# Performance work log

Measured on AMD Instinct MI355X. Metric: run time of the kernel, lower is better.

## Reference

```python
import jax, jax.numpy as jnp
import numpy as np

N, F, E = 10000, 128, 640000
HID_RO = 64


def setup_inputs() -> dict:
    key = jax.random.key(0)
    ks = jax.random.split(key, 16)
    s = 1.0 / np.sqrt(F)
    inp = {
        'h': jax.random.normal(ks[0], (N, F), jnp.float32),
        'src_idx': jax.random.randint(ks[1], (E,), 0, N, jnp.int32),
        'dst_idx': jax.random.randint(ks[2], (E,), 0, N, jnp.int32),
        # message-creation MLP (F -> F -> F)
        'W1': jax.random.normal(ks[3], (F, F), jnp.float32) * s,
        'b1': jnp.zeros((F,), jnp.float32),
        'W2': jax.random.normal(ks[4], (F, F), jnp.float32) * s,
        'b2': jnp.zeros((F,), jnp.float32),
        # attention aggregation kernels
        'node_kernel': jax.random.normal(ks[5], (F, F), jnp.float32) * s,
        'attn_kernel': jax.random.normal(ks[6], (2 * F, 1), jnp.float32) * s,
        # feed-forward update (agg + h -> new h)
        'Wu': jax.random.normal(ks[7], (2 * F, F), jnp.float32) * s,
        'bu': jnp.zeros((F,), jnp.float32),
        # readout MLP (F -> 64 -> 1)
        'Wr1': jax.random.normal(ks[8], (F, HID_RO), jnp.float32) * s,
        'br1': jnp.zeros((HID_RO,), jnp.float32),
        'Wr2': jax.random.normal(ks[9], (HID_RO, 1), jnp.float32) * (1.0 / np.sqrt(HID_RO)),
        'br2': jnp.zeros((1,), jnp.float32),
    }
    return inp


def reference(h, src_idx, dst_idx, W1, b1, W2, b2, node_kernel, attn_kernel,
              Wu, bu, Wr1, br1, Wr2, br2):
    n = h.shape[0]
    # per-edge gather + message-creation NN  [E, F]
    h_src = h[src_idx]
    m = jax.nn.relu(h_src @ W1 + b1) @ W2 + b2
    # attention aggregation (GAT-style): transform messages, score vs dst state
    wh = m @ node_kernel                      # [E, F]
    h_dst = h[dst_idx]                        # [E, F]
    e = jax.nn.leaky_relu(jnp.concatenate([wh, h_dst], axis=-1) @ attn_kernel,
                          negative_slope=0.2)[:, 0]  # [E]
    # per-destination segment softmax (numerically stable)
    e_max = jax.ops.segment_max(e, dst_idx, num_segments=n)
    ex = jnp.exp(e - e_max[dst_idx])
    denom = jax.ops.segment_sum(ex, dst_idx, num_segments=n)
    alpha = ex / (denom[dst_idx] + 1e-9)
    # scatter-reduce weighted messages into destination states  [N, F]
    agg = jax.ops.segment_sum(m * alpha[:, None], dst_idx, num_segments=n)
    # feed-forward update
    h_new = jax.nn.relu(jnp.concatenate([agg, h], axis=-1) @ Wu + bu)
    # readout MLP -> per-node scalar
    out = jax.nn.relu(h_new @ Wr1 + br1) @ Wr2 + br2  # [N, 1]
    return out
```

## Files before the change

### kernel.cpp

```cpp
#include <hip/hip_runtime.h>
#include <hip/hip_bf16.h>
#include <hip/hip_fp16.h>

#define F 128
#define HID 64
#define KMAX 4
#define DEG_CAP 256
#define NTM 16
#define NTU 16
#define CHUNK_LOG 13
#define CHUNK (1 << CHUNK_LOG)


__global__ __launch_bounds__(256) void fused_front(
    const int* __restrict__ dst, unsigned short* __restrict__ cnt,
    unsigned short* __restrict__ rank,
    int e, int n, int histBlocks,
    const float* __restrict__ h,
    const float* __restrict__ W1, const float* __restrict__ b1,
    const float* __restrict__ W2, const float* __restrict__ b2,
    const float* __restrict__ nk, const float* __restrict__ attn,
    __half* __restrict__ Mh, float* __restrict__ p, float* __restrict__ q)
{
    __shared__ __align__(16) int lhist[10240];
    int tid = threadIdx.x;

    if ((int)blockIdx.x < histBlocks) {
        int n4 = n >> 2;
        int4* lh4 = (int4*)lhist;
        for (int i = tid; i < n4; i += 256) lh4[i] = make_int4(0, 0, 0, 0);
        for (int i = (n4 << 2) + tid; i < n; i += 256) lhist[i] = 0;
        __syncthreads();

        int base = (int)blockIdx.x << CHUNK_LOG;
        int lim = min(e - base, CHUNK);
        int lim4 = lim >> 2;
        const int4* d4 = (const int4*)(dst + base);
        for (int k = tid; k < lim4; k += 256) {
            int4 dv = d4[k];
            ushort4 rv;
            rv.x = (unsigned short)atomicAdd(&lhist[dv.x], 1);
            rv.y = (unsigned short)atomicAdd(&lhist[dv.y], 1);
            rv.z = (unsigned short)atomicAdd(&lhist[dv.z], 1);
            rv.w = (unsigned short)atomicAdd(&lhist[dv.w], 1);
            *(ushort4*)&rank[base + 4 * k] = rv;
        }
        for (int k = (lim4 << 2) + tid; k < lim; k += 256)
            rank[base + k] = (unsigned short)atomicAdd(&lhist[dst[base + k]], 1);
        __syncthreads();

        unsigned int* crow = (unsigned int*)(cnt + (size_t)blockIdx.x * n);
        int nh = n >> 1;
        for (int i = tid; i < nh; i += 256) {
            unsigned int v = ((unsigned int)lhist[2 * i] & 0xffffu) |
                             ((unsigned int)lhist[2 * i + 1] << 16);
            crow[i] = v;
        }
        return;
    }

    float* smem = (float*)lhist;
    int bm = blockIdx.x - histBlocks;
    int row0 = bm * NTM;
    int wv   = tid >> 6;
    int lane = tid & 63;
    int j0 = (lane & 31) * 4;
    int rh = (lane >> 5) * 8;

    #pragma unroll
    for (int it = 0; it < 2; ++it) {
        int s4 = tid + it * 256;
        int r = s4 >> 5, c4 = s4 & 31;
        int row = row0 + r;
        float4 v = make_float4(0, 0, 0, 0);
        if (row < n) v = *(const float4*)&h[(size_t)row * F + c4 * 4];
        *(float4*)&smem[r * F + c4 * 4] = v;
    }
    __syncthreads();

    {
        int r = tid >> 4, kp = tid & 15;
        float qa = 0.f;
        #pragma unroll
        for (int c = 0; c < 2; ++c) {
            float4 hv = *(const float4*)&smem[r * F + kp * 8 + c * 4];
            float4 av = *(const float4*)&attn[F + kp * 8 + c * 4];
            qa = fmaf(hv.x, av.x, qa); qa = fmaf(hv.y, av.y, qa);
            qa = fmaf(hv.z, av.z, qa); qa = fmaf(hv.w, av.w, qa);
        }
        #pragma unroll
        for (int off = 1; off < 16; off <<= 1) qa += __shfl_xor(qa, off, 64);
        int row = row0 + r;
        if (kp == 0 && row < n) q[row] = qa;
    }

    float4 acc[8];
    #pragma unroll
    for (int i = 0; i < 8; ++i) acc[i] = make_float4(0.f, 0.f, 0.f, 0.f);
    int kbase = wv * 32;
    for (int k4 = 0; k4 < 8; ++k4) {
        int kk = kbase + k4 * 4;
        float4 a[8];
        #pragma unroll
        for (int r = 0; r < 8; ++r) a[r] = *(const float4*)&smem[(rh + r) * F + kk];
        #pragma unroll
        for (int k = 0; k < 4; ++k) {
            float4 b = *(const float4*)&W1[(size_t)(kk + k) * F + j0];
            #pragma unroll
            for (int r = 0; r < 8; ++r) {
                float av = k == 0 ? a[r].x : k == 1 ? a[r].y : k == 2 ? a[r].z : a[r].w;
                acc[r].x = fmaf(av, b.x, acc[r].x);
                acc[r].y = fmaf(av, b.y, acc[r].y);
                acc[r].z = fmaf(av, b.z, acc[r].z);
                acc[r].w = fmaf(av, b.w, acc[r].w);
            }
        }
    }
    __syncthreads();

    #pragma unroll
    for (int r = 0; r < 8; ++r)
        *(float4*)&smem[2048 + wv * 2048 + (rh + r) * 128 + j0] = acc[r];
    __syncthreads();

    #pragma unroll
    for (int u = 0; u < 2; ++u) {
        int idx = tid * 2 + u;
        int row = idx >> 5, c4 = (idx & 31) * 4;
        float4 s0 = *(const float4*)&smem[2048 + 0 * 2048 + row * 128 + c4];
        float4 s1 = *(const float4*)&smem[2048 + 1 * 2048 + row * 128 + c4];
        float4 s2 = *(const float4*)&smem[2048 + 2 * 2048 + row * 128 + c4];
        float4 s3 = *(const float4*)&smem[2048 + 3 * 2048 + row * 128 + c4];
        float4 bv = *(const float4*)&b1[c4];
        float4 t;
        t.x = fmaxf(s0.x + s1.x + s2.x + s3.x + bv.x, 0.f);
        t.y = fmaxf(s0.y + s1.y + s2.y + s3.y + bv.y, 0.f);
        t.z = fmaxf(s0.z + s1.z + s2.z + s3.z + bv.z, 0.f);
        t.w = fmaxf(s0.w + s1.w + s2.w + s3.w + bv.w, 0.f);
        *(float4*)&smem[row * 128 + c4] = t;
    }
    __syncthreads();

    #pragma unroll
    for (int i = 0; i < 8; ++i) acc[i] = make_float4(0.f, 0.f, 0.f, 0.f);
    for (int k4 = 0; k4 < 8; ++k4) {
        int kk = kbase + k4 * 4;
        float4 a[8];
        #pragma unroll
        for (int r = 0; r < 8; ++r) a[r] = *(const float4*)&smem[(rh + r) * 128 + kk];
        #pragma unroll
        for (int k = 0; k < 4; ++k) {
            float4 b = *(const float4*)&W2[(size_t)(kk + k) * F + j0];
            #pragma unroll
            for (int r = 0; r < 8; ++r) {
                float av = k == 0 ? a[r].x : k == 1 ? a[r].y : k == 2 ? a[r].z : a[r].w;
                acc[r].x = fmaf(av, b.x, acc[r].x);
                acc[r].y = fmaf(av, b.y, acc[r].y);
                acc[r].z = fmaf(av, b.z, acc[r].z);
                acc[r].w = fmaf(av, b.w, acc[r].w);
            }
        }
    }
    __syncthreads();
    #pragma unroll
    for (int r = 0; r < 8; ++r)
        *(float4*)&smem[2048 + wv * 2048 + (rh + r) * 128 + j0] = acc[r];
    __syncthreads();

    #pragma unroll
    for (int u = 0; u < 2; ++u) {
        int idx = tid * 2 + u;
        int row = idx >> 5, c4 = (idx & 31) * 4;
        float4 s0 = *(const float4*)&smem[2048 + 0 * 2048 + row * 128 + c4];
        float4 s1 = *(const float4*)&smem[2048 + 1 * 2048 + row * 128 + c4];
        float4 s2 = *(const float4*)&smem[2048 + 2 * 2048 + row * 128 + c4];
        float4 s3 = *(const float4*)&smem[2048 + 3 * 2048 + row * 128 + c4];
        float4 bv = *(const float4*)&b2[c4];
        float4 t;
        t.x = s0.x + s1.x + s2.x + s3.x + bv.x;
        t.y = s0.y + s1.y + s2.y + s3.y + bv.y;
        t.z = s0.z + s1.z + s2.z + s3.z + bv.z;
        t.w = s0.w + s1.w + s2.w + s3.w + bv.w;
        *(float4*)&smem[row * 128 + c4] = t;
    }
    __syncthreads();

    if (tid < F) {
        float a = 0.f;
        const float4* nkr = (const float4*)&nk[(size_t)tid * F];
        const float4* at4 = (const float4*)attn;
        #pragma unroll 8
        for (int j = 0; j < 32; ++j) {
            float4 nv = nkr[j]; float4 av = at4[j];
            a = fmaf(nv.x, av.x, a); a = fmaf(nv.y, av.y, a);
            a = fmaf(nv.z, av.z, a); a = fmaf(nv.w, av.w, a);
        }
        smem[2048 + tid] = a;
    }
    __syncthreads();

    {
        int row = tid >> 4, c8 = (tid & 15) * 8;
        int grow = row0 + row;
        float4 m0 = *(const float4*)&smem[row * 128 + c8];
        float4 m1 = *(const float4*)&smem[row * 128 + c8 + 4];
        if (grow < n) {
            __half hv[8];
            hv[0] = __float2half(m0.x); hv[1] = __float2half(m0.y);
            hv[2] = __float2half(m0.z); hv[3] = __float2half(m0.w);
            hv[4] = __float2half(m1.x); hv[5] = __float2half(m1.y);
            hv[6] = __float2half(m1.z); hv[7] = __float2half(m1.w);
            *(uint4*)&Mh[(size_t)grow * F + c8] = *(uint4*)hv;
        }
        float4 v0 = *(const float4*)&smem[2048 + c8];
        float4 v1v = *(const float4*)&smem[2048 + c8 + 4];
        float pp = m0.x * v0.x + m0.y * v0.y + m0.z * v0.z + m0.w * v0.w +
                   m1.x * v1v.x + m1.y * v1v.y + m1.z * v1v.z + m1.w * v1v.w;
        #pragma unroll
        for (int off = 1; off < 16; off <<= 1) pp += __shfl_xor(pp, off, 64);
        if ((tid & 15) == 0 && grow < n) p[grow] = pp;
    }
}

__global__ __launch_bounds__(256) void scan_block(
    unsigned short* __restrict__ cnt, int* __restrict__ rstart,
    int* __restrict__ bsum, int n, int hb)
{
    int tid = threadIdx.x;
    int i = blockIdx.x * 256 + tid;
    int run = 0;
    if (i < n) {
        size_t stride = (size_t)n;
        size_t idx = (size_t)i;
        int r = 0;
        for (; r + 8 <= hb; r += 8) {
            int c0 = cnt[idx];
            int c1 = cnt[idx + stride];
            int c2 = cnt[idx + 2 * stride];
            int c3 = cnt[idx + 3 * stride];
            int c4 = cnt[idx + 4 * stride];
            int c5 = cnt[idx + 5 * stride];
            int c6 = cnt[idx + 6 * stride];
            int c7 = cnt[idx + 7 * stride];
            cnt[idx]              = (unsigned short)run;
            cnt[idx + stride]     = (unsigned short)(run + c0);
            cnt[idx + 2 * stride] = (unsigned short)(run + (c0 + c1));
            cnt[idx + 3 * stride] = (unsigned short)(run + (c0 + c1 + c2));
            cnt[idx + 4 * stride] = (unsigned short)(run + (c0 + c1 + c2 + c3));
            cnt[idx + 5 * stride] = (unsigned short)(run + (c0 + c1 + c2 + c3 + c4));
            cnt[idx + 6 * stride] = (unsigned short)(run + (c0 + c1 + c2 + c3 + c4 + c5));
            cnt[idx + 7 * stride] = (unsigned short)(run + (c0 + c1 + c2 + c3 + c4 + c5 + c6));
            run += c0 + c1 + c2 + c3 + c4 + c5 + c6 + c7;
            idx += 8 * stride;
        }
        for (; r < hb; ++r) {
            int c = cnt[idx];
            cnt[idx] = (unsigned short)run;
            run += c;
            idx += stride;
        }
    }
    int v = run;
    int lane = tid & 63, wv = tid >> 6;
    int x = v;
    #pragma unroll
    for (int off = 1; off < 64; off <<= 1) {
        int t = __shfl_up(x, off, 64);
        if (lane >= off) x += t;
    }
    __shared__ int wsum[4];
    if (lane == 63) wsum[wv] = x;
    __syncthreads();
    int woff = 0;
    #pragma unroll
    for (int wdx = 0; wdx < 4; ++wdx) woff += (wdx < wv) ? wsum[wdx] : 0;
    int incl = x + woff;
    if (i < n) rstart[i] = incl - v;
    if (tid == 255) bsum[blockIdx.x] = incl;
}

__global__ __launch_bounds__(256) void fill_kernel(
    const int* __restrict__ dst, const int* __restrict__ src,
    const unsigned short* __restrict__ rank, const int* __restrict__ rstart,
    const unsigned short* __restrict__ cntoff, const int* __restrict__ bsum,
    unsigned short* __restrict__ src_sorted, int n, int nb, int e)
{
    __shared__ int sbo[64];
    int tid = threadIdx.x;
    if (tid < 64) {
        int v = (tid < nb) ? bsum[tid] : 0;
        int x = v;
        #pragma unroll
        for (int off = 1; off < 64; off <<= 1) {
            int t = __shfl_up(x, off, 64);
            if (tid >= off) x += t;
        }
        sbo[tid] = x - v;
    }
    __syncthreads();
    int i = blockIdx.x * 256 + tid;
    if (i < e) {
        int d = dst[i];
        int rep = i >> CHUNK_LOG;
        int pos = rstart[d] + sbo[d >> 8] + (int)cntoff[(size_t)rep * n + d] + (int)rank[i];
        src_sorted[pos] = (unsigned short)src[i];
    }
}

__global__ __launch_bounds__(256) void agg_update(
    const __half* __restrict__ Mh, const float* __restrict__ p,
    const float* __restrict__ q, const int* __restrict__ rstart,
    const int* __restrict__ bsum, const unsigned short* __restrict__ src_sorted,
    const float* __restrict__ h,
    const float* __restrict__ Wu, const float* __restrict__ bu,
    const float* __restrict__ Wr1, const float* __restrict__ br1,
    const float* __restrict__ Wr2, const float* __restrict__ br2,
    float* __restrict__ out, int n, int nb, int e)
{
    __shared__ __align__(16) float smem[8192];
    float (*X)[2 * F] = (float (*)[2 * F])smem;
    int2* bufa = (int2*)&smem[4096];
    int*  sbo  = (int*)&smem[6144];

    int tid = threadIdx.x;
    int wv   = tid >> 6;
    int lane = tid & 63;
    int row0 = blockIdx.x * NTU;

    if (tid < 64) {
        int v = (tid < nb) ? bsum[tid] : 0;
        int x = v;
        #pragma unroll
        for (int off = 1; off < 64; off <<= 1) {
            int t = __shfl_up(x, off, 64);
            if (tid >= off) x += t;
        }
        sbo[tid] = x - v;
    }
    #pragma unroll
    for (int it = 0; it < 2; ++it) {
        int s4 = tid + it * 256;
        int r = s4 >> 5, c4 = s4 & 31;
        int row = row0 + r;
        float4 v = make_float4(0, 0, 0, 0);
        if (row < n) v = *(const float4*)&h[(size_t)row * F + c4 * 4];
        *(float4*)&X[r][128 + c4 * 4] = v;
    }
    __syncthreads();

    const uint4* M16 = (const uint4*)Mh;
    int sub16 = lane & 15;
    int quar  = lane >> 4;
    int2* bufw = bufa + wv * DEG_CAP;

    for (int s = 0; s < 4; ++s) {
        int lr = wv * 4 + s;
        int node = row0 + lr;
        if (node >= n) break;

        int start = rstart[node] + sbo[node >> 8];
        int end   = (node + 1 < n) ? rstart[node + 1] + sbo[(node + 1) >> 8] : e;
        int deg   = end - start;
        float qn  = q[node];

        float w[KMAX];
        int   sidx[KMAX];
        float lmax = -1e30f;

        #pragma unroll
        for (int k = 0; k < KMAX; ++k) {
            int i = start + lane + (k << 6);
            bool valid = (i < end);
            int sv = valid ? (int)src_sorted[i] : 0;
            float pv = valid ? p[sv] : 0.0f;
            float sc = pv + qn;
            float ev = (sc > 0.0f) ? sc : 0.2f * sc;
            w[k] = valid ? ev : -1e30f;
            sidx[k] = sv;
            lmax = fmaxf(lmax, w[k]);
        }
        for (int i = start + DEG_CAP + lane; i < end; i += 64) {
            float sc = p[(int)src_sorted[i]] + qn;
            float ev = (sc > 0.0f) ? sc : 0.2f * sc;
            lmax = fmaxf(lmax, ev);
        }
        #pragma unroll
        for (int off = 32; off >= 1; off >>= 1)
            lmax = fmaxf(lmax, __shfl_xor(lmax, off, 64));

        float lsum = 0.0f;
        #pragma unroll
        for (int k = 0; k < KMAX; ++k) {
            float ex = (w[k] > -1e29f) ? __expf(w[k] - lmax) : 0.0f;
            w[k] = ex;
            lsum += ex;
        }
        for (int i = start + DEG_CAP + lane; i < end; i += 64) {
            float sc = p[(int)src_sorted[i]] + qn;
            float ev = (sc > 0.0f) ? sc : 0.2f * sc;
            lsum += __expf(ev - lmax);
        }
        #pragma unroll
        for (int off = 32; off >= 1; off >>= 1)
            lsum += __shfl_xor(lsum, off, 64);
        float inv = 1.0f / (lsum + 1e-9f);

        #pragma unroll
        for (int k = 0; k < KMAX; ++k)
            bufw[lane + (k << 6)] = make_int2(__float_as_int(w[k] * inv), sidx[k]);

        float acc[8] = {0.f, 0.f, 0.f, 0.f, 0.f, 0.f, 0.f, 0.f};
        int lim = min(deg, DEG_CAP);
        lim = (lim + 15) & ~15;

        for (int base = 0; base < lim; base += 16) {
            int2  rr[4];
            uint4 mm[4];
            #pragma unroll
            for (int u = 0; u < 4; ++u) rr[u] = bufw[base + quar + 4 * u];
            #pragma unroll
            for (int u = 0; u < 4; ++u) mm[u] = M16[(size_t)rr[u].y * 16 + sub16];
            #pragma unroll
            for (int u = 0; u < 4; ++u) {
                float wu = __int_as_float(rr[u].x);
                const __half2* hp = (const __half2*)&mm[u];
                float2 f0 = __half22float2(hp[0]);
                float2 f1 = __half22float2(hp[1]);
                float2 f2 = __half22float2(hp[2]);
                float2 f3 = __half22float2(hp[3]);
                acc[0] = fmaf(wu, f0.x, acc[0]); acc[1] = fmaf(wu, f0.y, acc[1]);
                acc[2] = fmaf(wu, f1.x, acc[2]); acc[3] = fmaf(wu, f1.y, acc[3]);
                acc[4] = fmaf(wu, f2.x, acc[4]); acc[5] = fmaf(wu, f2.y, acc[5]);
                acc[6] = fmaf(wu, f3.x, acc[6]); acc[7] = fmaf(wu, f3.y, acc[7]);
            }
        }

        for (int base = start + DEG_CAP; base < end; base += 64) {
            int i = base + lane;
            float ex = 0.f; int sv = 0;
            if (i < end) {
                sv = (int)src_sorted[i];
                float sc = p[sv] + qn;
                float ev = (sc > 0.0f) ? sc : 0.2f * sc;
                ex = __expf(ev - lmax) * inv;
            }
            bufw[lane] = make_int2(__float_as_int(ex), sv);
            for (int b2 = 0; b2 < 64; b2 += 4) {
                int2 rr = bufw[b2 + quar];
                uint4 mm = M16[(size_t)rr.y * 16 + sub16];
                float wu = __int_as_float(rr.x);
                const __half2* hp = (const __half2*)&mm;
                float2 f0 = __half22float2(hp[0]);
                float2 f1 = __half22float2(hp[1]);
                float2 f2 = __half22float2(hp[2]);
                float2 f3 = __half22float2(hp[3]);
                acc[0] = fmaf(wu, f0.x, acc[0]); acc[1] = fmaf(wu, f0.y, acc[1]);
                acc[2] = fmaf(wu, f1.x, acc[2]); acc[3] = fmaf(wu, f1.y, acc[3]);
                acc[4] = fmaf(wu, f2.x, acc[4]); acc[5] = fmaf(wu, f2.y, acc[5]);
                acc[6] = fmaf(wu, f3.x, acc[6]); acc[7] = fmaf(wu, f3.y, acc[7]);
            }
        }

        #pragma unroll
        for (int j = 0; j < 8; ++j) {
            acc[j] += __shfl_xor(acc[j], 16, 64);
            acc[j] += __shfl_xor(acc[j], 32, 64);
        }
        if (quar == 0) {
            *(float4*)&X[lr][sub16 * 8]     = make_float4(acc[0], acc[1], acc[2], acc[3]);
            *(float4*)&X[lr][sub16 * 8 + 4] = make_float4(acc[4], acc[5], acc[6], acc[7]);
        }
    }
    __syncthreads();

    int j0 = (lane & 31) * 4;
    int rh = (lane >> 5) * 8;
    float4 acc[8];
    #pragma unroll
    for (int i = 0; i < 8; ++i) acc[i] = make_float4(0.f, 0.f, 0.f, 0.f);
    int kbase = wv * 64;
    for (int k4 = 0; k4 < 16; ++k4) {
        int kk = kbase + k4 * 4;
        float4 a[8];
        #pragma unroll
        for (int r = 0; r < 8; ++r) a[r] = *(const float4*)&X[rh + r][kk];
        #pragma unroll
        for (int k = 0; k < 4; ++k) {
            float4 b = *(const float4*)&Wu[(size_t)(kk + k) * F + j0];
            #pragma unroll
            for (int r = 0; r < 8; ++r) {
                float av = k == 0 ? a[r].x : k == 1 ? a[r].y : k == 2 ? a[r].z : a[r].w;
                acc[r].x = fmaf(av, b.x, acc[r].x);
                acc[r].y = fmaf(av, b.y, acc[r].y);
                acc[r].z = fmaf(av, b.z, acc[r].z);
                acc[r].w = fmaf(av, b.w, acc[r].w);
            }
        }
    }
    __syncthreads();

    #pragma unroll
    for (int r = 0; r < 8; ++r)
        *(float4*)&smem[wv * 2048 + (rh + r) * 128 + j0] = acc[r];
    __syncthreads();

    #pragma unroll
    for (int u = 0; u < 2; ++u) {
        int idx = tid * 2 + u;
        int row = idx >> 5, c4 = (idx & 31) * 4;
        float4 s0 = *(const float4*)&smem[0 * 2048 + row * 128 + c4];
        float4 s1 = *(const float4*)&smem[1 * 2048 + row * 128 + c4];
        float4 s2 = *(const float4*)&smem[2 * 2048 + row * 128 + c4];
        float4 s3 = *(const float4*)&smem[3 * 2048 + row * 128 + c4];
        float4 bv = *(const float4*)&bu[c4];
        float4 t;
        t.x = fmaxf(s0.x + s1.x + s2.x + s3.x + bv.x, 0.f);
        t.y = fmaxf(s0.y + s1.y + s2.y + s3.y + bv.y, 0.f);
        t.z = fmaxf(s0.z + s1.z + s2.z + s3.z + bv.z, 0.f);
        t.w = fmaxf(s0.w + s1.w + s2.w + s3.w + bv.w, 0.f);
        *(float4*)&smem[row * 128 + c4] = t;
    }
    __syncthreads();

    int h0 = (lane & 31) * 2;
    float r1a[8], r1b[8];
    #pragma unroll
    for (int r = 0; r < 8; ++r) { r1a[r] = 0.f; r1b[r] = 0.f; }
    int kb2 = wv * 32;
    for (int k4 = 0; k4 < 8; ++k4) {
        int kk = kb2 + k4 * 4;
        float4 a[8];
        #pragma unroll
        for (int r = 0; r < 8; ++r) a[r] = *(const float4*)&smem[(rh + r) * 128 + kk];
        #pragma unroll
        for (int k = 0; k < 4; ++k) {
            float2 b = *(const float2*)&Wr1[(size_t)(kk + k) * HID + h0];
            #pragma unroll
            for (int r = 0; r < 8; ++r) {
                float av = k == 0 ? a[r].x : k == 1 ? a[r].y : k == 2 ? a[r].z : a[r].w;
                r1a[r] = fmaf(av, b.x, r1a[r]);
                r1b[r] = fmaf(av, b.y, r1b[r]);
            }
        }
    }
    #pragma unroll
    for (int r = 0; r < 8; ++r) {
        smem[2048 + wv * 1024 + (rh + r) * 64 + h0]     = r1a[r];
        smem[2048 + wv * 1024 + (rh + r) * 64 + h0 + 1] = r1b[r];
    }
    __syncthreads();

    {
        int row = tid >> 4;
        int hp  = (tid & 15) * 4;
        float val = 0.f;
        #pragma unroll
        for (int j = 0; j < 4; ++j) {
            int hh = hp + j;
            float s = br1[hh]
                    + smem[2048 + 0 * 1024 + row * 64 + hh]
                    + smem[2048 + 1 * 1024 + row * 64 + hh]
                    + smem[2048 + 2 * 1024 + row * 64 + hh]
                    + smem[2048 + 3 * 1024 + row * 64 + hh];
            val = fmaf(fmaxf(s, 0.f), Wr2[hh], val);
        }
        #pragma unroll
        for (int off = 1; off < 16; off <<= 1) val += __shfl_xor(val, off, 64);
        int orow = row0 + row;
        if ((tid & 15) == 0 && orow < n) out[orow] = val + br2[0];
    }
}

extern "C" void kernel_launch(void* const* d_in, const int* in_sizes, int n_in,
                              void* d_out, int out_size, void* d_ws, size_t ws_size,
                              hipStream_t stream) {
    const float* h    = (const float*)d_in[0];
    const int*   src  = (const int*)d_in[1];
    const int*   dst  = (const int*)d_in[2];
    const float* W1   = (const float*)d_in[3];
    const float* b1   = (const float*)d_in[4];
    const float* W2   = (const float*)d_in[5];
    const float* b2   = (const float*)d_in[6];
    const float* nk   = (const float*)d_in[7];
    const float* attn = (const float*)d_in[8];
    const float* Wu   = (const float*)d_in[9];
    const float* bu   = (const float*)d_in[10];
    const float* Wr1  = (const float*)d_in[11];
    const float* br1  = (const float*)d_in[12];
    const float* Wr2  = (const float*)d_in[13];
    const float* br2  = (const float*)d_in[14];
    float* out = (float*)d_out;

    int n = in_sizes[0] / F;
    int e = in_sizes[1];
    int nb = (n + 255) / 256;
    int hb = (e + CHUNK - 1) >> CHUNK_LOG;
    int mlpBlocks  = (n + NTM - 1) / NTM;
    int fusBlocks  = (n + NTU - 1) / NTU;
    int fillBlocks = (e + 255) / 256;

    char* ws = (char*)d_ws;
    size_t off = 0;
    auto alloc = [&](size_t bytes) {
        void* pp = ws + off;
        off += (bytes + 511) & ~(size_t)511;
        return pp;
    };
    __half* Mh             = (__half*)alloc((size_t)n * F * 2);
    float* p               = (float*)alloc((size_t)n * 4);
    float* q               = (float*)alloc((size_t)n * 4);
    unsigned short* cnt    = (unsigned short*)alloc((size_t)hb * n * 2);
    int*   rstart          = (int*)alloc((size_t)(n + 1) * 4);
    int*   bsum            = (int*)alloc((size_t)(nb + 1) * 4);
    unsigned short* rank   = (unsigned short*)alloc((size_t)e * 2);
    unsigned short* srcsort= (unsigned short*)alloc((size_t)e * 2);

    fused_front<<<hb + mlpBlocks, 256, 0, stream>>>(
        dst, cnt, rank, e, n, hb,
        h, W1, b1, W2, b2, nk, attn, Mh, p, q);
    scan_block<<<nb, 256, 0, stream>>>(cnt, rstart, bsum, n, hb);
    fill_kernel<<<fillBlocks, 256, 0, stream>>>(dst, src, rank, rstart,
                                                cnt, bsum, srcsort,
                                                n, nb, e);
    agg_update<<<fusBlocks, 256, 0, stream>>>(Mh, p, q, rstart, bsum, srcsort,
                                              h, Wu, bu, Wr1, br1, Wr2, br2,
                                              out, n, nb, e);
}
```

Before: 154.5 us.

## Split per-node histogram scan across four thread groups and double chunk size

The scan kernel now uses 1024 threads per block, with four groups each summing a quarter of the histogram rows for the same 256 nodes. The groups combine partial sums through shared memory, then each rewrites its rows as exclusive offsets. CHUNK_LOG is also raised, which halves the number of histogram blocks and so the number of count rows to scan. The aim is to shorten the long serial row loop per thread in the scan. The cost is an extra pass over the counts and larger chunks in the front histogram stage, which may reduce parallelism there.

After: 152.3 us, median of 2. No clear change (-1.4%).

```diff
diff --git a/kernel.cpp b/kernel.cpp
--- a/kernel.cpp
+++ b/kernel.cpp
@@ -8,7 +8,7 @@
 #define DEG_CAP 256
 #define NTM 16
 #define NTU 16
-#define CHUNK_LOG 13
+#define CHUNK_LOG 14
 #define CHUNK (1 << CHUNK_LOG)
 
 
@@ -222,61 +222,72 @@
     }
 }
 
-__global__ __launch_bounds__(256) void scan_block(
+__global__ __launch_bounds__(1024) void scan_block(
     unsigned short* __restrict__ cnt, int* __restrict__ rstart,
     int* __restrict__ bsum, int n, int hb)
 {
+    __shared__ int psum[4][256];
+    __shared__ int wsum[4];
     int tid = threadIdx.x;
-    int i = blockIdx.x * 256 + tid;
-    int run = 0;
+    int ln = tid & 255, g = tid >> 8;
+    int i = blockIdx.x * 256 + ln;
+    int per = (hb + 3) >> 2;
+    int r0 = g * per, r1 = min(hb, r0 + per);
+
+    int s = 0;
     if (i < n) {
-        size_t stride = (size_t)n;
-        size_t idx = (size_t)i;
-        int r = 0;
-        for (; r + 8 <= hb; r += 8) {
+        size_t idx = (size_t)r0 * n + i;
+        int r = r0;
+        for (; r + 4 <= r1; r += 4) {
             int c0 = cnt[idx];
-            int c1 = cnt[idx + stride];
-            int c2 = cnt[idx + 2 * stride];
-            int c3 = cnt[idx + 3 * stride];
-            int c4 = cnt[idx + 4 * stride];
-            int c5 = cnt[idx + 5 * stride];
-            int c6 = cnt[idx + 6 * stride];
-            int c7 = cnt[idx + 7 * stride];
-            cnt[idx]              = (unsigned short)run;
-            cnt[idx + stride]     = (unsigned short)(run + c0);
-            cnt[idx + 2 * stride] = (unsigned short)(run + (c0 + c1));
-            cnt[idx + 3 * stride] = (unsigned short)(run + (c0 + c1 + c2));
-            cnt[idx + 4 * stride] = (unsigned short)(run + (c0 + c1 + c2 + c3));
-            cnt[idx + 5 * stride] = (unsigned short)(run + (c0 + c1 + c2 + c3 + c4));
-            cnt[idx + 6 * stride] = (unsigned short)(run + (c0 + c1 + c2 + c3 + c4 + c5));
-            cnt[idx + 7 * stride] = (unsigned short)(run + (c0 + c1 + c2 + c3 + c4 + c5 + c6));
-            run += c0 + c1 + c2 + c3 + c4 + c5 + c6 + c7;
-            idx += 8 * stride;
-        }
-        for (; r < hb; ++r) {
+            int c1 = cnt[idx + (size_t)n];
+            int c2 = cnt[idx + 2 * (size_t)n];
+            int c3 = cnt[idx + 3 * (size_t)n];
+            s += c0 + c1 + c2 + c3;
+            idx += 4 * (size_t)n;
+        }
+        for (; r < r1; ++r) { s += cnt[idx]; idx += n; }
+    }
+    psum[g][ln] = s;
+    __syncthreads();
+
+    int base = 0;
+    #pragma unroll
+    for (int gg = 0; gg < 3; ++gg) base += (gg < g) ? psum[gg][ln] : 0;
+    int tot = psum[0][ln] + psum[1][ln] + psum[2][ln] + psum[3][ln];
+
+    if (i < n) {
+        size_t idx = (size_t)r0 * n + i;
+        int run = base;
+        for (int r = r0; r < r1; ++r) {
             int c = cnt[idx];
             cnt[idx] = (unsigned short)run;
             run += c;
-            idx += stride;
-        }
-    }
-    int v = run;
-    int lane = tid & 63, wv = tid >> 6;
-    int x = v;
-    #pragma unroll
-    for (int off = 1; off < 64; off <<= 1) {
-        int t = __shfl_up(x, off, 64);
-        if (lane >= off) x += t;
-    }
-    __shared__ int wsum[4];
-    if (lane == 63) wsum[wv] = x;
-    __syncthreads();
-    int woff = 0;
-    #pragma unroll
-    for (int wdx = 0; wdx < 4; ++wdx) woff += (wdx < wv) ? wsum[wdx] : 0;
-    int incl = x + woff;
-    if (i < n) rstart[i] = incl - v;
-    if (tid == 255) bsum[blockIdx.x] = incl;
+            idx += n;
+        }
+    }
+
+    int lane = ln & 63, wv4 = ln >> 6;
+    int x = 0, v = 0;
+    if (g == 0) {
+        v = (i < n) ? tot : 0;
+        x = v;
+        #pragma unroll
+        for (int off = 1; off < 64; off <<= 1) {
+            int t = __shfl_up(x, off, 64);
+            if (lane >= off) x += t;
+        }
+        if (lane == 63) wsum[wv4] = x;
+    }
+    __syncthreads();
+    if (g == 0) {
+        int woff = 0;
+        #pragma unroll
+        for (int wdx = 0; wdx < 4; ++wdx) woff += (wdx < wv4) ? wsum[wdx] : 0;
+        int incl = x + woff;
+        if (i < n) rstart[i] = incl - v;
+        if (ln == 255) bsum[blockIdx.x] = incl;
+    }
 }
 
 __global__ __launch_bounds__(256) void fill_kernel(
@@ -618,7 +629,7 @@
     fused_front<<<hb + mlpBlocks, 256, 0, stream>>>(
         dst, cnt, rank, e, n, hb,
         h, W1, b1, W2, b2, nk, attn, Mh, p, q);
-    scan_block<<<nb, 256, 0, stream>>>(cnt, rstart, bsum, n, hb);
+    scan_block<<<nb, 1024, 0, stream>>>(cnt, rstart, bsum, n, hb);
     fill_kernel<<<fillBlocks, 256, 0, stream>>>(dst, src, rank, rstart,
                                                 cnt, bsum, srcsort,
                                                 n, nb, e);
```
